# Kernel tuning notes

Hardware: AMD Instinct MI355X
Metric: run time of the kernel (lower is better)

The kernel has to match this reference:

```python
import jax, jax.numpy as jnp
import numpy as np

B, C = 16384, 1024
N_ITERS = 16


def _spectral_normalize(W):
    # SpectralNormLinear divides the weight by its largest singular value;
    # we bake that parametrization into the stored weight (forward math identical).
    s = np.linalg.svd(np.asarray(W), compute_uv=False)[0]
    return jnp.asarray(np.asarray(W) / s, dtype=jnp.float32)


def setup_inputs() -> dict:
    key = jax.random.key(0)
    ks = jax.random.split(key, 9)
    y = jax.random.normal(ks[0], (B, C), dtype=jnp.float32)
    log_det_jacobians = jnp.zeros((B,), dtype=jnp.float32)
    v = jax.random.normal(ks[1], (B, C), dtype=jnp.float32)  # Hutchinson probe (n_samples=1)
    def mk_w(k):
        W = jax.random.normal(k, (C, C), dtype=jnp.float32) / np.sqrt(C).astype(np.float32)
        return _spectral_normalize(W)
    W1, W2, W3 = mk_w(ks[2]), mk_w(ks[3]), mk_w(ks[4])
    b1 = jax.random.normal(ks[5], (C,), dtype=jnp.float32) * 0.01
    b2 = jax.random.normal(ks[6], (C,), dtype=jnp.float32) * 0.01
    b3 = jax.random.normal(ks[7], (C,), dtype=jnp.float32) * 0.01
    return {"y": y, "log_det_jacobians": log_det_jacobians, "v": v,
            "W1": W1, "b1": b1, "W2": W2, "b2": b2, "W3": W3, "b3": b3}


def reference(y, log_det_jacobians, v, W1, b1, W2, b2, W3, b3):
    def mlp(x):  # SpectralNormLinear -> ELU -> SpectralNormLinear -> ELU -> SpectralNormLinear
        h = jax.nn.elu(x @ W1.T + b1)
        h = jax.nn.elu(h @ W2.T + b2)
        return h @ W3.T + b3

    g_y, vjp_fn = jax.vjp(mlp, y)  # residuals reused across all 16 power iterations

    def body(carry, k):
        w, acc = carry
        w = vjp_fn(w)[0]                     # w <- J^T w  (torch.autograd.grad step)
        inner = jnp.sum(w * v, axis=-1)      # einsum('bnd,bnd->bn') with n_samples=1
        # torch: if (k+1) % 2 == 0 (k odd): +inner/k else -inner/k
        sign = jnp.where(jnp.mod(k, 2.0) == 1.0, 1.0, -1.0)
        acc = acc + sign * inner / k
        return (w, acc), None

    ks = jnp.arange(1, N_ITERS + 1, dtype=jnp.float32)
    (_, log_det_J), _ = jax.lax.scan(body, (v, jnp.zeros_like(log_det_jacobians)), ks)

    z = y + g_y
    # torch.mean over n_samples dim is identity for n_samples=1
    return z, log_det_jacobians + log_det_J
```

## Files before the change

kernel.cpp:

```cpp
#include <hip/hip_runtime.h>
#include <cmath>

#define BROWS 16384
#define CDIM  1024
#define NIT   16

typedef __attribute__((ext_vector_type(8))) short short8;
typedef __attribute__((ext_vector_type(4))) short short4v;
typedef __attribute__((ext_vector_type(4))) float floatx4;

__device__ __forceinline__ unsigned short f2bf(float f) {
  union { float f; unsigned u; } x; x.f = f;
  unsigned r = x.u + 0x7fffu + ((x.u >> 16) & 1u);
  return (unsigned short)(r >> 16);
}
__device__ __forceinline__ float bf2f(unsigned short h) {
  union { float f; unsigned u; } x; x.u = ((unsigned)h) << 16;
  return x.f;
}

__global__ void prep_weights(const float* __restrict__ W1, const float* __restrict__ W2,
                             const float* __restrict__ W3,
                             unsigned short* __restrict__ Wb, unsigned short* __restrict__ Wt) {
  int idx = blockIdx.x * 256 + threadIdx.x;
  int m = idx >> 20;
  int r = (idx >> 10) & 1023;
  int c = idx & 1023;
  const float* W = (m == 0) ? W1 : ((m == 1) ? W2 : W3);
  unsigned short b = f2bf(W[r * CDIM + c]);
  Wb[idx] = b;
  Wt[(m << 20) + c * CDIM + r] = b;
}

__global__ void conv_inputs(const float* __restrict__ y, const float* __restrict__ v,
                            unsigned short* __restrict__ ybf, unsigned short* __restrict__ vbf,
                            float* __restrict__ inner) {
  int i = (blockIdx.x * 256 + threadIdx.x) * 4;
  floatx4 yv = *(const floatx4*)(y + i);
  floatx4 vv = *(const floatx4*)(v + i);
  short4v a, b;
#pragma unroll
  for (int r = 0; r < 4; r++) { a[r] = (short)f2bf(yv[r]); b[r] = (short)f2bf(vv[r]); }
  *(short4v*)(ybf + i) = a;
  *(short4v*)(vbf + i) = b;
  if (i < NIT * BROWS) *(floatx4*)(inner + i) = floatx4{0.f, 0.f, 0.f, 0.f};
}

template <int MODE>
__global__ __launch_bounds__(512, 2)
void gemm_k(const unsigned short* __restrict__ A,
            const unsigned short* __restrict__ Bm,
            const float* __restrict__ bias,
            const float* __restrict__ yin,
            const unsigned short* __restrict__ Dm,
            const unsigned short* __restrict__ vin,
            unsigned short* __restrict__ outB,
            float* __restrict__ outZ,
            float* __restrict__ inner) {
  constexpr int K = CDIM;
  __shared__ unsigned short smem[65536];

  const int t = threadIdx.x;
  const int wg = (gridDim.x == 256) ? ((blockIdx.x & 7) * 32 + (blockIdx.x >> 3))
                                    : blockIdx.x;
  const int m0 = (wg >> 2) * 256;
  const int n0 = (wg & 3) * 256;

  const int wave = t >> 6, lane = t & 63;
  const int quad = lane >> 4, ln = lane & 15;
  const int wm = wave >> 2;
  const int wn = wave & 3;

  const int srow = t >> 3;
  const int gcolE = ((t & 7) ^ (srow & 7)) * 8;
  const unsigned short* gA = A + (size_t)(m0 + srow) * K + gcolE;
  const unsigned short* gB = Bm + (size_t)(n0 + srow) * K + gcolE;
  const int ldE = t * 8;

  const int swzE = (ln & 7) << 3;
  const int aHalf = wm * 8192;
  const int bHalf = 16384 + (wn >> 1) * 8192;
  const int bRow = (wn & 1) * 64;

#define GLL(gp, le)                                                                       \
  __builtin_amdgcn_global_load_lds((const __attribute__((address_space(1))) void*)(gp),   \
                                   (__attribute__((address_space(3))) void*)&smem[le], 16, 0, 0)
#define STAGE_A1(k0, pb) do {                                                             \
    GLL(gA + (k0),                    (pb) + ldE);                                        \
    GLL(gA + (size_t)128 * K + (k0),  (pb) + 8192 + ldE);                                 \
  } while (0)
#define STAGE_A2(k0, pb) do {                                                             \
    GLL(gA + (size_t)64 * K + (k0),   (pb) + 4096 + ldE);                                 \
    GLL(gA + (size_t)192 * K + (k0),  (pb) + 8192 + 4096 + ldE);                          \
  } while (0)
#define STAGE_B2a(k0, pb) do {                                                            \
    GLL(gB + (k0),                    (pb) + 16384 + ldE);                                \
    GLL(gB + (size_t)64 * K + (k0),   (pb) + 16384 + 4096 + ldE);                         \
  } while (0)
#define STAGE_B2b(k0, pb) do {                                                            \
    GLL(gB + (size_t)128 * K + (k0),  (pb) + 16384 + 8192 + ldE);                         \
    GLL(gB + (size_t)192 * K + (k0),  (pb) + 16384 + 8192 + 4096 + ldE);                  \
  } while (0)

  floatx4 acc[8][4];
#pragma unroll
  for (int i = 0; i < 8; ++i)
#pragma unroll
    for (int j = 0; j < 4; ++j) acc[i][j] = {0.f, 0.f, 0.f, 0.f};

  short8 aF[4][2];
  short8 bF[4][2];

  STAGE_A1(0, 0); STAGE_B2a(0, 0); STAGE_B2b(0, 0); STAGE_A2(0, 0);
  asm volatile("s_waitcnt vmcnt(2)" ::: "memory");
  __builtin_amdgcn_s_barrier();

#define READ_A(qm_, bufE_) do {                                                           \
    _Pragma("unroll") for (int mi = 0; mi < 4; ++mi)                                      \
    _Pragma("unroll") for (int ks = 0; ks < 2; ++ks)                                      \
      aF[mi][ks] = *(const short8*)&smem[(bufE_) + aHalf + ((qm_) * 64 + mi * 16 + ln) * 64 \
                                         + ((ks * 32 + quad * 8) ^ swzE)];                \
  } while (0)
#define READ_B2(n0_, bufE_) do {                                                          \
    _Pragma("unroll") for (int ni = (n0_); ni < (n0_) + 2; ++ni)                          \
    _Pragma("unroll") for (int ks = 0; ks < 2; ++ks)                                      \
      bF[ni][ks] = *(const short8*)&smem[(bufE_) + bHalf + (bRow + ni * 16 + ln) * 64     \
                                         + ((ks * 32 + quad * 8) ^ swzE)];                \
  } while (0)
#define MFMA_Q(qm_, qn_) do {                                                             \
    _Pragma("unroll") for (int mi = 0; mi < 4; ++mi)                                      \
    _Pragma("unroll") for (int ni = 0; ni < 2; ++ni)                                      \
    _Pragma("unroll") for (int ks = 0; ks < 2; ++ks)                                      \
      acc[(qm_) * 4 + mi][(qn_) * 2 + ni] = __builtin_amdgcn_mfma_f32_16x16x32_bf16(      \
          aF[mi][ks], bF[(qn_) * 2 + ni][ks], acc[(qm_) * 4 + mi][(qn_) * 2 + ni], 0, 0, 0); \
  } while (0)

#pragma unroll 2
  for (int kt = 0; kt < 16; ++kt) {
    const int bufE = (kt & 1) * 32768;
    const int nxtE = bufE ^ 32768;
    const int kn = (kt + 1) * 64;
    const bool st = (kt < 15);

    READ_A(0, bufE);
    READ_B2(0, bufE);
    if (st) { STAGE_A1(kn, nxtE); STAGE_B2a(kn, nxtE); }
    __builtin_amdgcn_s_barrier();
    asm volatile("s_waitcnt lgkmcnt(0)" ::: "memory");
    __builtin_amdgcn_sched_barrier(0);
    __builtin_amdgcn_s_setprio(1);
    READ_B2(2, bufE);
    MFMA_Q(0, 0);
    __builtin_amdgcn_s_setprio(0);
    __builtin_amdgcn_sched_barrier(0);
    __builtin_amdgcn_s_barrier();

    if (st) STAGE_B2b(kn, nxtE);
    __builtin_amdgcn_s_barrier();
    if (kt == 15) asm volatile("s_waitcnt vmcnt(0)" ::: "memory");
    else          asm volatile("s_waitcnt vmcnt(6)" ::: "memory");
    asm volatile("s_waitcnt lgkmcnt(0)" ::: "memory");
    __builtin_amdgcn_sched_barrier(0);
    __builtin_amdgcn_s_setprio(1);
    MFMA_Q(0, 1);
    READ_A(1, bufE);
    __builtin_amdgcn_s_setprio(0);
    __builtin_amdgcn_sched_barrier(0);
    __builtin_amdgcn_s_barrier();

    if (st) STAGE_A2(kn, nxtE);
    __builtin_amdgcn_s_barrier();
    asm volatile("s_waitcnt lgkmcnt(0)" ::: "memory");
    __builtin_amdgcn_sched_barrier(0);
    __builtin_amdgcn_s_setprio(1);
    MFMA_Q(1, 0);
    __builtin_amdgcn_s_setprio(0);
    __builtin_amdgcn_sched_barrier(0);
    __builtin_amdgcn_s_barrier();

    __builtin_amdgcn_s_barrier();
    __builtin_amdgcn_s_setprio(1);
    MFMA_Q(1, 1);
    __builtin_amdgcn_s_setprio(0);
    __builtin_amdgcn_sched_barrier(0);
    if (st) asm volatile("s_waitcnt vmcnt(2)" ::: "memory");
    __builtin_amdgcn_s_barrier();
  }
#undef MFMA_Q
#undef READ_A
#undef READ_B2
#undef STAGE_A1
#undef STAGE_A2
#undef STAGE_B2a
#undef STAGE_B2b
#undef GLL

  unsigned short* Ct = smem;
  const int colW = wn * 64 + ln;
  float bv[4];
  if (MODE == 0) {
#pragma unroll
    for (int NI = 0; NI < 4; ++NI) bv[NI] = bias[n0 + colW + NI * 16];
  }
  for (int h = 0; h < 2; ++h) {
    if (wm == h) {
#pragma unroll
      for (int MI = 0; MI < 8; ++MI)
#pragma unroll
        for (int NI = 0; NI < 4; ++NI)
#pragma unroll
          for (int r = 0; r < 4; ++r) {
            float pv = acc[MI][NI][r];
            if (MODE == 0) {
              pv += bv[NI];
              pv = (pv > 0.f) ? pv : expm1f(pv);
            }
            Ct[(MI * 16 + quad * 4 + r) * 260 + colW + NI * 16] = f2bf(pv);
          }
    }
    __syncthreads();
    const int rr = t >> 5;
    const int cc = (t & 31) * 8;
#pragma unroll
    for (int it = 0; it < 8; ++it) {
      const int lr = it * 16 + rr;
      short4v v0 = *(const short4v*)&Ct[lr * 260 + cc];
      short4v v1 = *(const short4v*)&Ct[lr * 260 + cc + 4];
      short8 val;
#pragma unroll
      for (int i = 0; i < 4; ++i) { val[i] = v0[i]; val[i + 4] = v1[i]; }
      const size_t o = (size_t)(m0 + h * 128 + lr) * CDIM + (n0 + cc);
      if (MODE == 0) {
        *(short8*)&outB[o] = val;
      } else if (MODE == 1) {
        const floatx4 y0 = *(const floatx4*)&yin[o];
        const floatx4 y1 = *(const floatx4*)&yin[o + 4];
        const floatx4 b0 = *(const floatx4*)&bias[n0 + cc];
        const floatx4 b1 = *(const floatx4*)&bias[n0 + cc + 4];
        floatx4 z0, z1;
#pragma unroll
        for (int i = 0; i < 4; ++i) {
          z0[i] = bf2f((unsigned short)val[i]) + b0[i] + y0[i];
          z1[i] = bf2f((unsigned short)val[i + 4]) + b1[i] + y1[i];
        }
        *(floatx4*)&outZ[o] = z0;
        *(floatx4*)&outZ[o + 4] = z1;
      } else if (MODE == 2) {
        short8 d = *(const short8*)&Dm[o];
        short8 ov;
#pragma unroll
        for (int i = 0; i < 8; ++i) {
          float dp = fminf(bf2f((unsigned short)d[i]) + 1.f, 1.f);
          ov[i] = (short)f2bf(bf2f((unsigned short)val[i]) * dp);
        }
        *(short8*)&outB[o] = ov;
      } else if (MODE == 3) {
        short8 d = *(const short8*)&Dm[o];
        short8 vv = *(const short8*)&vin[o];
        short8 ov;
        float ps = 0.f;
#pragma unroll
        for (int i = 0; i < 8; ++i) {
          float dp = fminf(bf2f((unsigned short)d[i]) + 1.f, 1.f);
          float pu = bf2f((unsigned short)val[i]) * dp;
          ov[i] = (short)f2bf(pu);
          ps += pu * bf2f((unsigned short)vv[i]);
        }
        *(short8*)&outB[o] = ov;
        ps += __shfl_xor(ps, 1);
        ps += __shfl_xor(ps, 2);
        ps += __shfl_xor(ps, 4);
        ps += __shfl_xor(ps, 8);
        ps += __shfl_xor(ps, 16);
        if ((t & 31) == 0) atomicAdd(&inner[m0 + h * 128 + lr], ps);
      } else {
        *(short8*)&outB[o] = val;
      }
    }
    __syncthreads();
  }
}

__global__ void combine_ldj(const float* __restrict__ ldj_in, const float* __restrict__ inner,
                            float* __restrict__ out) {
  int b = blockIdx.x * 256 + threadIdx.x;
  if (b < BROWS) {
    float a = ldj_in[b];
#pragma unroll
    for (int k = 1; k <= NIT; k++) {
      float s = (k & 1) ? 1.f : -1.f;
      a += s * inner[(k - 1) * BROWS + b] / (float)k;
    }
    out[b] = a;
  }
}

extern "C" void kernel_launch(void* const* d_in, const int* in_sizes, int n_in,
                              void* d_out, int out_size, void* d_ws, size_t ws_size,
                              hipStream_t stream) {
  const float* y   = (const float*)d_in[0];
  const float* ldj = (const float*)d_in[1];
  const float* v   = (const float*)d_in[2];
  const float* W1  = (const float*)d_in[3];
  const float* b1  = (const float*)d_in[4];
  const float* W2  = (const float*)d_in[5];
  const float* b2  = (const float*)d_in[6];
  const float* W3  = (const float*)d_in[7];
  const float* b3  = (const float*)d_in[8];

  float* z_out   = (float*)d_out;
  float* ldj_out = z_out + (size_t)BROWS * CDIM;

  const size_t MC = (size_t)BROWS * CDIM;
  const size_t WW = (size_t)3 * CDIM * CDIM;
  unsigned short* Wb    = (unsigned short*)d_ws;
  unsigned short* Wt    = Wb + WW;
  float*          inner = (float*)(Wt + WW);
  unsigned short* ybf   = (unsigned short*)(inner + NIT * BROWS);
  unsigned short* ua    = ybf + MC;
  unsigned short* ub    = ua + MC;
  unsigned short* vb    = ub + MC;
  unsigned short* h1    = vb + MC;
  unsigned short* h2    = h1 + MC;
  unsigned short* M13   = h2 + MC;

  prep_weights<<<(3 * CDIM * CDIM) / 256, 256, 0, stream>>>(W1, W2, W3, Wb, Wt);
  conv_inputs<<<(BROWS * CDIM) / (256 * 4), 256, 0, stream>>>(y, v, ybf, vb, inner);

  dim3 grid(256);
  dim3 gridW(16);

  gemm_k<4><<<gridW, 512, 0, stream>>>(Wt + (2 << 20), Wb, nullptr, nullptr, nullptr, nullptr, M13, nullptr, nullptr);

  gemm_k<0><<<grid, 512, 0, stream>>>(ybf, Wb,             b1, nullptr, nullptr, nullptr, h1, nullptr, nullptr);
  gemm_k<4><<<grid, 512, 0, stream>>>(vb,  Wb,             nullptr, nullptr, nullptr, nullptr, ybf, nullptr, nullptr);
  gemm_k<0><<<grid, 512, 0, stream>>>(h1,  Wb + (1 << 20), b2, nullptr, nullptr, nullptr, h2, nullptr, nullptr);
  gemm_k<1><<<grid, 512, 0, stream>>>(h2,  Wb + (2 << 20), b3, y,       nullptr, nullptr, nullptr, z_out, nullptr);

  gemm_k<2><<<grid, 512, 0, stream>>>(vb, Wt + (2 << 20), nullptr, nullptr, h2, nullptr, ua, nullptr, nullptr);
  for (int k = 1; k <= NIT; k++) {
    gemm_k<3><<<grid, 512, 0, stream>>>(ua, Wt + (1 << 20), nullptr, nullptr, h1, ybf, ub, nullptr, inner + (size_t)(k - 1) * BROWS);
    if (k < NIT)
      gemm_k<2><<<grid, 512, 0, stream>>>(ub, M13, nullptr, nullptr, h2, nullptr, ua, nullptr, nullptr);
  }

  combine_ldj<<<(BROWS + 255) / 256, 256, 0, stream>>>(ldj, inner, ldj_out);
}
```

Measured before the change: 1.793 ms.

## Add small-tile weight GEMM, drop redundant LDS waits, skip final iteration store

Adds a dedicated 128x128-tile kernel that precomputes the fused W1·W3 weight product over 64 workgroups, replacing the 16-workgroup launch of the big GEMM kernel. The main GEMM's tile mapping is fixed to the swizzled form, and three explicit lgkmcnt(0) waits are removed from the pipelined k-loop. A new MODE 5 is used for the last power iteration so it only accumulates the inner product and does not write an output matrix nobody reads. Removing the LDS waits relies on the compiler inserting the needed waits itself, which is a correctness and scheduling risk.

Result: faster. 1.725 ms (-3.8%).

```diff
diff --git a/kernel.cpp b/kernel.cpp
--- a/kernel.cpp
+++ b/kernel.cpp
@@ -44,6 +44,94 @@
   *(short4v*)(ybf + i) = a;
   *(short4v*)(vbf + i) = b;
   if (i < NIT * BROWS) *(floatx4*)(inner + i) = floatx4{0.f, 0.f, 0.f, 0.f};
+}
+
+__global__ __launch_bounds__(256, 2)
+void gemm_w(const unsigned short* __restrict__ A, const unsigned short* __restrict__ Bm,
+            unsigned short* __restrict__ outB) {
+  constexpr int K = CDIM;
+  __shared__ unsigned short smem[32768];
+  const int t = threadIdx.x;
+  const int m0 = (blockIdx.x >> 3) * 128;
+  const int n0 = (blockIdx.x & 7) * 128;
+  const int wave = t >> 6, lane = t & 63;
+  const int quad = lane >> 4, ln = lane & 15;
+  const int wm = wave >> 1, wn = wave & 1;
+  const int srow = t >> 3;
+  const int gcolE = ((t & 7) ^ (srow & 7)) * 8;
+  const unsigned short* gA = A + (size_t)(m0 + srow) * K + gcolE;
+  const unsigned short* gB = Bm + (size_t)(n0 + srow) * K + gcolE;
+  const int ldE = t * 8;
+  const int swzE = (ln & 7) << 3;
+
+#define GLLW(gp, le)                                                                      \
+  __builtin_amdgcn_global_load_lds((const __attribute__((address_space(1))) void*)(gp),   \
+                                   (__attribute__((address_space(3))) void*)&smem[le], 16, 0, 0)
+#define STAGEW(k0, pb) do {                                                               \
+    _Pragma("unroll") for (int g = 0; g < 4; ++g) {                                       \
+      GLLW(gA + (size_t)(g * 32) * K + (k0), (pb) + g * 2048 + ldE);                      \
+      GLLW(gB + (size_t)(g * 32) * K + (k0), (pb) + 8192 + g * 2048 + ldE);               \
+    }                                                                                     \
+  } while (0)
+
+  floatx4 acc[4][4];
+#pragma unroll
+  for (int i = 0; i < 4; ++i)
+#pragma unroll
+    for (int j = 0; j < 4; ++j) acc[i][j] = {0.f, 0.f, 0.f, 0.f};
+
+  STAGEW(0, 0);
+  for (int kt = 0; kt < 16; ++kt) {
+    const int cb = (kt & 1) * 16384;
+    __syncthreads();
+    if (kt < 15) STAGEW((kt + 1) * 64, cb ^ 16384);
+    short8 aF[4][2], bF[4][2];
+#pragma unroll
+    for (int mi = 0; mi < 4; ++mi)
+#pragma unroll
+      for (int ks = 0; ks < 2; ++ks)
+        aF[mi][ks] = *(const short8*)&smem[cb + (wm * 64 + mi * 16 + ln) * 64
+                                           + ((ks * 32 + quad * 8) ^ swzE)];
+#pragma unroll
+    for (int ni = 0; ni < 4; ++ni)
+#pragma unroll
+      for (int ks = 0; ks < 2; ++ks)
+        bF[ni][ks] = *(const short8*)&smem[cb + 8192 + (wn * 64 + ni * 16 + ln) * 64
+                                           + ((ks * 32 + quad * 8) ^ swzE)];
+#pragma unroll
+    for (int mi = 0; mi < 4; ++mi)
+#pragma unroll
+      for (int ni = 0; ni < 4; ++ni)
+#pragma unroll
+        for (int ks = 0; ks < 2; ++ks)
+          acc[mi][ni] = __builtin_amdgcn_mfma_f32_16x16x32_bf16(aF[mi][ks], bF[ni][ks],
+                                                                acc[mi][ni], 0, 0, 0);
+  }
+  __syncthreads();
+
+  unsigned short* Ct = smem;
+#pragma unroll
+  for (int mi = 0; mi < 4; ++mi)
+#pragma unroll
+    for (int ni = 0; ni < 4; ++ni)
+#pragma unroll
+      for (int r = 0; r < 4; ++r)
+        Ct[(wm * 64 + mi * 16 + quad * 4 + r) * 132 + wn * 64 + ln + ni * 16] =
+            f2bf(acc[mi][ni][r]);
+  __syncthreads();
+  const int rr = t >> 4, cc = (t & 15) * 8;
+#pragma unroll
+  for (int it = 0; it < 8; ++it) {
+    const int lr = it * 16 + rr;
+    short4v v0 = *(const short4v*)&Ct[lr * 132 + cc];
+    short4v v1 = *(const short4v*)&Ct[lr * 132 + cc + 4];
+    short8 val;
+#pragma unroll
+    for (int i = 0; i < 4; ++i) { val[i] = v0[i]; val[i + 4] = v1[i]; }
+    *(short8*)&outB[(size_t)(m0 + lr) * CDIM + (n0 + cc)] = val;
+  }
+#undef STAGEW
+#undef GLLW
 }
 
 template <int MODE>
@@ -61,8 +149,7 @@
   __shared__ unsigned short smem[65536];
 
   const int t = threadIdx.x;
-  const int wg = (gridDim.x == 256) ? ((blockIdx.x & 7) * 32 + (blockIdx.x >> 3))
-                                    : blockIdx.x;
+  const int wg = (blockIdx.x & 7) * 32 + (blockIdx.x >> 3);
   const int m0 = (wg >> 2) * 256;
   const int n0 = (wg & 3) * 256;
 
@@ -146,7 +233,6 @@
     READ_B2(0, bufE);
     if (st) { STAGE_A1(kn, nxtE); STAGE_B2a(kn, nxtE); }
     __builtin_amdgcn_s_barrier();
-    asm volatile("s_waitcnt lgkmcnt(0)" ::: "memory");
     __builtin_amdgcn_sched_barrier(0);
     __builtin_amdgcn_s_setprio(1);
     READ_B2(2, bufE);
@@ -159,7 +245,6 @@
     __builtin_amdgcn_s_barrier();
     if (kt == 15) asm volatile("s_waitcnt vmcnt(0)" ::: "memory");
     else          asm volatile("s_waitcnt vmcnt(6)" ::: "memory");
-    asm volatile("s_waitcnt lgkmcnt(0)" ::: "memory");
     __builtin_amdgcn_sched_barrier(0);
     __builtin_amdgcn_s_setprio(1);
     MFMA_Q(0, 1);
@@ -170,7 +255,6 @@
 
     if (st) STAGE_A2(kn, nxtE);
     __builtin_amdgcn_s_barrier();
-    asm volatile("s_waitcnt lgkmcnt(0)" ::: "memory");
     __builtin_amdgcn_sched_barrier(0);
     __builtin_amdgcn_s_setprio(1);
     MFMA_Q(1, 0);
@@ -254,7 +338,7 @@
           ov[i] = (short)f2bf(bf2f((unsigned short)val[i]) * dp);
         }
         *(short8*)&outB[o] = ov;
-      } else if (MODE == 3) {
+      } else if (MODE == 3 || MODE == 5) {
         short8 d = *(const short8*)&Dm[o];
         short8 vv = *(const short8*)&vin[o];
         short8 ov;
@@ -266,7 +350,7 @@
           ov[i] = (short)f2bf(pu);
           ps += pu * bf2f((unsigned short)vv[i]);
         }
-        *(short8*)&outB[o] = ov;
+        if (MODE == 3) *(short8*)&outB[o] = ov;
         ps += __shfl_xor(ps, 1);
         ps += __shfl_xor(ps, 2);
         ps += __shfl_xor(ps, 4);
@@ -328,9 +412,8 @@
   conv_inputs<<<(BROWS * CDIM) / (256 * 4), 256, 0, stream>>>(y, v, ybf, vb, inner);
 
   dim3 grid(256);
-  dim3 gridW(16);
-
-  gemm_k<4><<<gridW, 512, 0, stream>>>(Wt + (2 << 20), Wb, nullptr, nullptr, nullptr, nullptr, M13, nullptr, nullptr);
+
+  gemm_w<<<64, 256, 0, stream>>>(Wt + (2 << 20), Wb, M13);
 
   gemm_k<0><<<grid, 512, 0, stream>>>(ybf, Wb,             b1, nullptr, nullptr, nullptr, h1, nullptr, nullptr);
   gemm_k<4><<<grid, 512, 0, stream>>>(vb,  Wb,             nullptr, nullptr, nullptr, nullptr, ybf, nullptr, nullptr);
@@ -338,11 +421,11 @@
   gemm_k<1><<<grid, 512, 0, stream>>>(h2,  Wb + (2 << 20), b3, y,       nullptr, nullptr, nullptr, z_out, nullptr);
 
   gemm_k<2><<<grid, 512, 0, stream>>>(vb, Wt + (2 << 20), nullptr, nullptr, h2, nullptr, ua, nullptr, nullptr);
-  for (int k = 1; k <= NIT; k++) {
+  for (int k = 1; k <= NIT - 1; k++) {
     gemm_k<3><<<grid, 512, 0, stream>>>(ua, Wt + (1 << 20), nullptr, nullptr, h1, ybf, ub, nullptr, inner + (size_t)(k - 1) * BROWS);
-    if (k < NIT)
-      gemm_k<2><<<grid, 512, 0, stream>>>(ub, M13, nullptr, nullptr, h2, nullptr, ua, nullptr, nullptr);
-  }
+    gemm_k<2><<<grid, 512, 0, stream>>>(ub, M13, nullptr, nullptr, h2, nullptr, ua, nullptr, nullptr);
+  }
+  gemm_k<5><<<grid, 512, 0, stream>>>(ua, Wt + (1 << 20), nullptr, nullptr, h1, ybf, nullptr, nullptr, inner + (size_t)(NIT - 1) * BROWS);
 
   combine_ldj<<<(BROWS + 255) / 256, 256, 0, stream>>>(ldj, inner, ldj_out);
 }
```
